# Kernel optimization log

Hardware: AMD Instinct MI355X
Metric: run time of the kernel (lower is better)

The kernel has to match this reference:

```python
import jax, jax.numpy as jnp
import numpy as np

N, E, D_IN, D_H, D_OUT, L = 100000, 300000, 128, 128, 3, 12


def _gconv(x, edges, W0, b0, W1, b1):
    # pytorch3d GraphConv: w0(x) + gather_scatter(w1(x), edges)
    y = x @ W0.T + b0                      # [N, D_out] self transform
    n = x @ W1.T + b1                      # [N, D_out] neighbor transform
    # undirected: each edge (i, j) adds n[j] to out[i] and n[i] to out[j]
    agg = jnp.zeros_like(y)
    agg = agg.at[edges[:, 0]].add(n[edges[:, 1]])
    agg = agg.at[edges[:, 1]].add(n[edges[:, 0]])
    return y + agg


def setup_inputs() -> dict:
    key = jax.random.key(0)
    ks = jax.random.split(key, 20)

    def lin(k, out_d, in_d):
        s = 1.0 / np.sqrt(in_d)
        return jax.random.uniform(k, (out_d, in_d), jnp.float32, -s, s)

    def bias(k, out_d, in_d):
        s = 1.0 / np.sqrt(in_d)
        return jax.random.uniform(k, (out_d,), jnp.float32, -s, s)

    features = jax.random.normal(ks[0], (N, D_IN), jnp.float32)
    edges = jax.random.randint(ks[1], (E, 2), 0, N, dtype=jnp.int32)

    # first layer (in -> hidden)
    W0_1, b0_1 = lin(ks[2], D_H, D_IN), bias(ks[3], D_H, D_IN)
    W1_1, b1_1 = lin(ks[4], D_H, D_IN), bias(ks[5], D_H, D_IN)
    # 12 hidden layers (hidden -> hidden), stacked for lax.scan
    W0_h = jax.vmap(lambda k: lin(k, D_H, D_H))(jax.random.split(ks[6], L))
    b0_h = jax.vmap(lambda k: bias(k, D_H, D_H))(jax.random.split(ks[7], L))
    W1_h = jax.vmap(lambda k: lin(k, D_H, D_H))(jax.random.split(ks[8], L))
    b1_h = jax.vmap(lambda k: bias(k, D_H, D_H))(jax.random.split(ks[9], L))
    # last layer (hidden -> out)
    W0_l, b0_l = lin(ks[10], D_OUT, D_H), bias(ks[11], D_OUT, D_H)
    W1_l, b1_l = lin(ks[12], D_OUT, D_H), bias(ks[13], D_OUT, D_H)

    return {
        "features": features, "edges": edges,
        "W0_1": W0_1, "b0_1": b0_1, "W1_1": W1_1, "b1_1": b1_1,
        "W0_h": W0_h, "b0_h": b0_h, "W1_h": W1_h, "b1_h": b1_h,
        "W0_l": W0_l, "b0_l": b0_l, "W1_l": W1_l, "b1_l": b1_l,
    }


def reference(features, edges, W0_1, b0_1, W1_1, b1_1,
              W0_h, b0_h, W1_h, b1_h, W0_l, b0_l, W1_l, b1_l):
    x = jax.nn.relu(_gconv(features, edges, W0_1, b0_1, W1_1, b1_1))
    residual = x

    def step(x, p):
        W0, b0, W1, b1 = p
        return jax.nn.relu(_gconv(x, edges, W0, b0, W1, b1)), None

    x, _ = jax.lax.scan(step, x, (W0_h, b0_h, W1_h, b1_h))
    auxiliary = x
    vertices = _gconv(residual + x, edges, W0_l, b0_l, W1_l, b1_l)
    return vertices, auxiliary
```

## Files before the change

### kernel.cpp

```cpp
#include <hip/hip_runtime.h>
#include <hip/hip_bf16.h>

#define D 128
#define OSTR 136
#define CHUNK 12544

typedef float f32x4  __attribute__((ext_vector_type(4)));
typedef unsigned int u32x4 __attribute__((ext_vector_type(4)));
typedef __attribute__((ext_vector_type(8))) __bf16 bh8;

union UV { uint4 u; bh8 h; };

__device__ inline float bf2f(unsigned short u) {
    union { unsigned int i; float f; } x; x.i = ((unsigned int)u) << 16; return x.f;
}
__device__ inline unsigned short f2bf(float f) {
    union { float f; unsigned int i; } x; x.f = f;
    return (unsigned short)((x.i + 0x7fffu + ((x.i >> 16) & 1u)) >> 16);
}
__device__ inline unsigned int addb2(unsigned int ua, unsigned int ub) {
    union { unsigned int i; float f; } la, ha, lb, hb;
    la.i = ua << 16; ha.i = ua & 0xffff0000u;
    lb.i = ub << 16; hb.i = ub & 0xffff0000u;
    return ((unsigned int)f2bf(ha.f + hb.f) << 16) | f2bf(la.f + lb.f);
}

__global__ void k_hist(const int* __restrict__ edges, int E, int* __restrict__ deg) {
    int e = blockIdx.x * blockDim.x + threadIdx.x;
    if (e < E) {
        atomicAdd(&deg[edges[2 * e]], 1);
        atomicAdd(&deg[edges[2 * e + 1]], 1);
    }
}

__global__ void k_scan1(const int* __restrict__ deg, int n,
                        int* __restrict__ incl, int* __restrict__ bsum) {
    __shared__ int lds[1024];
    int t = threadIdx.x;
    int i = blockIdx.x * 1024 + t;
    int v = (i < n) ? deg[i] : 0;
    int cur = v;
    lds[t] = cur;
    __syncthreads();
    for (int off = 1; off < 1024; off <<= 1) {
        int add = (t >= off) ? lds[t - off] : 0;
        __syncthreads();
        cur += add;
        lds[t] = cur;
        __syncthreads();
    }
    if (i < n) incl[i] = cur;
    if (t == 1023) bsum[blockIdx.x] = cur;
}

__global__ void k_scan2(int* __restrict__ bsum, int nb) {
    __shared__ int lds[128];
    int t = threadIdx.x;
    int v = (t < nb) ? bsum[t] : 0;
    int cur = v;
    lds[t] = cur;
    __syncthreads();
    for (int off = 1; off < 128; off <<= 1) {
        int add = (t >= off) ? lds[t - off] : 0;
        __syncthreads();
        cur += add;
        lds[t] = cur;
        __syncthreads();
    }
    if (t < nb) bsum[t] = cur - v;
}

__global__ void k_scan3(const int* __restrict__ incl, const int* __restrict__ deg,
                        const int* __restrict__ bsum, int n, int twoE,
                        int* __restrict__ rowstart, int* __restrict__ cursor) {
    int i = blockIdx.x * blockDim.x + threadIdx.x;
    if (i < n) {
        int r = incl[i] - deg[i] + bsum[i >> 10];
        rowstart[i] = r;
        cursor[i] = r;
    }
    if (i == 0) rowstart[n] = twoE;
}

__global__ void k_fill(const int* __restrict__ edges, int E,
                       int* __restrict__ cursor, int* __restrict__ adj) {
    int e = blockIdx.x * blockDim.x + threadIdx.x;
    if (e < E) {
        int a = edges[2 * e], b = edges[2 * e + 1];
        adj[atomicAdd(&cursor[a], 1)] = b;
        adj[atomicAdd(&cursor[b], 1)] = a;
    }
}

__global__ void k_wprep(const float* __restrict__ W0_1, const float* __restrict__ W1_1,
                        const float* __restrict__ W0_h, const float* __restrict__ W1_h,
                        unsigned short* __restrict__ wb) {
    int idx = blockIdx.x * 256 + threadIdx.x;
    if (idx >= 13 * 2 * 128 * 128) return;
    int k = idx & 127;
    int o = (idx >> 7) & 127;
    int m = (idx >> 14) & 1;
    int l = idx >> 15;
    const float* src = (l == 0) ? (m ? W1_1 : W0_1)
                                : ((m ? W1_h : W0_h) + (size_t)(l - 1) * 16384);
    float v = src[o * 128 + k];
    int kk = m * 128 + k;
    wb[(size_t)l * 32768 + (kk >> 5) * 4096 + o * 32 + (kk & 31)] = f2bf(v);
}

__global__ void k_cvt(const float* __restrict__ in, unsigned short* __restrict__ out, int n4) {
    int i = blockIdx.x * blockDim.x + threadIdx.x;
    if (i >= n4) return;
    f32x4 v = *(const f32x4*)&in[(size_t)i * 4];
    unsigned short u[4];
    #pragma unroll
    for (int j = 0; j < 4; ++j) u[j] = f2bf(v[j]);
    *(uint2*)&out[(size_t)i * 4] = *(uint2*)u;
}

__global__ __launch_bounds__(256) void k_agg(
    const unsigned short* __restrict__ x, const int* __restrict__ rowstart,
    const int* __restrict__ adj, unsigned short* __restrict__ s, int n) {
    int node = (blockIdx.x & 7) * CHUNK + (blockIdx.x >> 3) * 4 + (threadIdx.x >> 6);
    int lane = threadIdx.x & 63;
    if (node >= n) return;
    int r0 = rowstart[node], r1 = rowstart[node + 1];
    int c  = lane & 31;
    int hi = lane >> 5;
    float aa0 = 0.f, aa1 = 0.f, aa2 = 0.f, aa3 = 0.f;
    for (int p = r0; p < r1; p += 8) {
        int q = p + (lane & 7);
        int idx = (q < r1) ? adj[q] : adj[r0];
        uint2 u[4];
        #pragma unroll
        for (int k = 0; k < 4; ++k) {
            int j = __shfl(idx, 2 * k + hi);
            u[k] = *(const uint2*)&x[(size_t)j * D + c * 4];
        }
        #pragma unroll
        for (int k = 0; k < 4; ++k) {
            if (p + 2 * k + hi < r1) {
                union { unsigned int i; float f; } t;
                t.i = u[k].x << 16;          aa0 += t.f;
                t.i = u[k].x & 0xffff0000u;  aa1 += t.f;
                t.i = u[k].y << 16;          aa2 += t.f;
                t.i = u[k].y & 0xffff0000u;  aa3 += t.f;
            }
        }
    }
    aa0 += __shfl_xor(aa0, 32);
    aa1 += __shfl_xor(aa1, 32);
    aa2 += __shfl_xor(aa2, 32);
    aa3 += __shfl_xor(aa3, 32);
    if (hi == 0) {
        uint2 o;
        o.x = ((unsigned int)f2bf(aa1) << 16) | f2bf(aa0);
        o.y = ((unsigned int)f2bf(aa3) << 16) | f2bf(aa2);
        *(uint2*)&s[(size_t)node * D + c * 4] = o;
    }
}

__global__ __launch_bounds__(256) void k_gemm(
    const unsigned short* __restrict__ x,
    const unsigned short* __restrict__ s,
    const unsigned short* __restrict__ wb,
    const float* __restrict__ b0, const float* __restrict__ b1,
    const int* __restrict__ deg,
    unsigned short* __restrict__ out,
    float* __restrict__ out32,
    const unsigned short* __restrict__ resid,
    unsigned short* __restrict__ zout,
    int n, int do_relu) {
    __shared__ __align__(16) unsigned short LDS[64 * OSTR];
    int node0 = (blockIdx.x & 7) * CHUNK + (blockIdx.x >> 3) * 64;
    if (node0 >= n) return;
    int t = threadIdx.x;
    int lane = t & 63;
    int wave = t >> 6;
    int wm = (wave >> 1) * 32;
    int wn = (wave & 1) * 64;
    int mlane = lane & 15;
    int quad = lane >> 4;

    f32x4 acc[2][4];
    #pragma unroll
    for (int i = 0; i < 2; ++i)
        #pragma unroll
        for (int j = 0; j < 4; ++j) acc[i][j] = (f32x4){0.f, 0.f, 0.f, 0.f};

    uint4 ra[2][2];
    bh8 rb[2][4];
    auto LDK = [&](int kc, int st) {
        const unsigned short* srcA = (kc < 4) ? x : s;
        int kbase = (kc & 3) * 32;
        #pragma unroll
        for (int i = 0; i < 2; ++i) {
            int g = node0 + wm + i * 16 + mlane;
            uint4 v = {0u, 0u, 0u, 0u};
            if (g < n) v = *(const uint4*)&srcA[(size_t)g * D + kbase + quad * 8];
            ra[st][i] = v;
        }
        #pragma unroll
        for (int j = 0; j < 4; ++j)
            rb[st][j] = *(const bh8*)&wb[(size_t)kc * 4096 + (wn + j * 16 + mlane) * 32 + quad * 8];
    };

    LDK(0, 0);
    #pragma unroll
    for (int kc = 0; kc < 8; ++kc) {
        int cs = kc & 1;
        if (kc < 7) LDK(kc + 1, cs ^ 1);
        bh8 a0, a1;
        { UV v; v.u = ra[cs][0]; a0 = v.h; }
        { UV v; v.u = ra[cs][1]; a1 = v.h; }
        #pragma unroll
        for (int j = 0; j < 4; ++j) {
            acc[0][j] = __builtin_amdgcn_mfma_f32_16x16x32_bf16(a0, rb[cs][j], acc[0][j], 0, 0, 0);
            acc[1][j] = __builtin_amdgcn_mfma_f32_16x16x32_bf16(a1, rb[cs][j], acc[1][j], 0, 0, 0);
        }
    }

    #pragma unroll
    for (int i = 0; i < 2; ++i) {
        int mrow = wm + i * 16 + quad * 4;
        #pragma unroll
        for (int j = 0; j < 4; ++j) {
            int nn = wn + j * 16 + mlane;
            float b0v = b0[nn], b1v = b1[nn];
            #pragma unroll
            for (int r = 0; r < 4; ++r) {
                int g = node0 + mrow + r;
                float dg = (g < n) ? (float)deg[g] : 0.f;
                float val = acc[i][j][r] + b0v + dg * b1v;
                if (do_relu) val = fmaxf(val, 0.f);
                LDS[(mrow + r) * OSTR + nn] = f2bf(val);
            }
        }
    }
    __syncthreads();
    #pragma unroll
    for (int pass = 0; pass < 4; ++pass) {
        int row = pass * 16 + (t >> 4);
        int seg = (t & 15) * 8;
        int g = node0 + row;
        if (g < n) {
            u32x4 v = *(const u32x4*)&LDS[row * OSTR + seg];
            *(u32x4*)&out[(size_t)g * D + seg] = v;
            if (zout) {
                u32x4 rr = *(const u32x4*)&resid[(size_t)g * D + seg];
                u32x4 zz;
                zz.x = addb2(v.x, rr.x);
                zz.y = addb2(v.y, rr.y);
                zz.z = addb2(v.z, rr.z);
                zz.w = addb2(v.w, rr.w);
                *(u32x4*)&zout[(size_t)g * D + seg] = zz;
            }
        }
    }
    if (out32) {
        #pragma unroll
        for (int pass = 0; pass < 8; ++pass) {
            int row = pass * 8 + (t >> 5);
            int seg = (t & 31) * 4;
            int g = node0 + row;
            if (g < n) {
                f32x4 v;
                #pragma unroll
                for (int j = 0; j < 4; ++j) v[j] = bf2f(LDS[row * OSTR + seg + j]);
                *(f32x4*)&out32[(size_t)g * D + seg] = v;
            }
        }
    }
}

__global__ __launch_bounds__(256) void k_lastagg(
    const unsigned short* __restrict__ z, const int* __restrict__ rowstart,
    const int* __restrict__ adj,
    const float* __restrict__ W0, const float* __restrict__ b0,
    const float* __restrict__ W1, const float* __restrict__ b1,
    float* __restrict__ vert, int n) {
    int node = blockIdx.x * 4 + (threadIdx.x >> 6);
    int lane = threadIdx.x & 63;
    if (node >= n) return;
    int r0 = rowstart[node], r1 = rowstart[node + 1];
    int c  = lane & 31;
    int hi = lane >> 5;
    float aa0 = 0.f, aa1 = 0.f, aa2 = 0.f, aa3 = 0.f;
    for (int p = r0; p < r1; p += 8) {
        int q = p + (lane & 7);
        int idx = (q < r1) ? adj[q] : adj[r0];
        uint2 u[4];
        #pragma unroll
        for (int k = 0; k < 4; ++k) {
            int j = __shfl(idx, 2 * k + hi);
            u[k] = *(const uint2*)&z[(size_t)j * D + c * 4];
        }
        #pragma unroll
        for (int k = 0; k < 4; ++k) {
            if (p + 2 * k + hi < r1) {
                union { unsigned int i; float f; } t;
                t.i = u[k].x << 16;          aa0 += t.f;
                t.i = u[k].x & 0xffff0000u;  aa1 += t.f;
                t.i = u[k].y << 16;          aa2 += t.f;
                t.i = u[k].y & 0xffff0000u;  aa3 += t.f;
            }
        }
    }
    aa0 += __shfl_xor(aa0, 32);
    aa1 += __shfl_xor(aa1, 32);
    aa2 += __shfl_xor(aa2, 32);
    aa3 += __shfl_xor(aa3, 32);
    uint2 zz = *(const uint2*)&z[(size_t)node * D + c * 4];
    float z0, z1, z2, z3;
    { union { unsigned int i; float f; } t;
      t.i = zz.x << 16;         z0 = t.f;
      t.i = zz.x & 0xffff0000u; z1 = t.f;
      t.i = zz.y << 16;         z2 = t.f;
      t.i = zz.y & 0xffff0000u; z3 = t.f; }
    float dg = (float)(r1 - r0);
    #pragma unroll
    for (int o = 0; o < 3; ++o) {
        f32x4 w0 = *(const f32x4*)&W0[o * D + 4 * c];
        f32x4 w1 = *(const f32x4*)&W1[o * D + 4 * c];
        float p = z0 * w0[0] + z1 * w0[1] + z2 * w0[2] + z3 * w0[3]
                + aa0 * w1[0] + aa1 * w1[1] + aa2 * w1[2] + aa3 * w1[3];
        p += __shfl_xor(p, 16);
        p += __shfl_xor(p, 8);
        p += __shfl_xor(p, 4);
        p += __shfl_xor(p, 2);
        p += __shfl_xor(p, 1);
        if (lane == 0) vert[(size_t)node * 3 + o] = p + b0[o] + dg * b1[o];
    }
}

extern "C" void kernel_launch(void* const* d_in, const int* in_sizes, int n_in,
                              void* d_out, int out_size, void* d_ws, size_t ws_size,
                              hipStream_t stream) {
    const float* features = (const float*)d_in[0];
    const int*   edges    = (const int*)d_in[1];
    const float* W0_1 = (const float*)d_in[2];
    const float* b0_1 = (const float*)d_in[3];
    const float* W1_1 = (const float*)d_in[4];
    const float* b1_1 = (const float*)d_in[5];
    const float* W0_h = (const float*)d_in[6];
    const float* b0_h = (const float*)d_in[7];
    const float* W1_h = (const float*)d_in[8];
    const float* b1_h = (const float*)d_in[9];
    const float* W0_l = (const float*)d_in[10];
    const float* b0_l = (const float*)d_in[11];
    const float* W1_l = (const float*)d_in[12];
    const float* b1_l = (const float*)d_in[13];

    const int N_ = 100000, E_ = 300000;
    float* vert = (float*)d_out;
    float* aux  = (float*)d_out + (size_t)N_ * 3;

    char* w = (char*)d_ws;
    auto alloc = [&](size_t bytes) {
        char* p = w;
        w += (bytes + 255) & ~(size_t)255;
        return p;
    };
    unsigned short* wb    = (unsigned short*)alloc((size_t)13 * 32768 * 2);
    unsigned short* xf    = (unsigned short*)alloc((size_t)N_ * D * 2);
    unsigned short* resid = (unsigned short*)alloc((size_t)N_ * D * 2);
    unsigned short* xa    = (unsigned short*)alloc((size_t)N_ * D * 2);
    unsigned short* xb    = (unsigned short*)alloc((size_t)N_ * D * 2);
    unsigned short* sb    = (unsigned short*)alloc((size_t)N_ * D * 2);
    int* deg    = (int*)alloc((size_t)N_ * 4);
    int* incl   = (int*)alloc((size_t)N_ * 4);
    int* rowst  = (int*)alloc((size_t)(N_ + 1) * 4);
    int* cursor = (int*)alloc((size_t)N_ * 4);
    int* bsum   = (int*)alloc(128 * 4);
    int* adj    = (int*)alloc((size_t)2 * E_ * 4);

    hipMemsetAsync(deg, 0, (size_t)N_ * 4, stream);
    k_hist<<<(E_ + 255) / 256, 256, 0, stream>>>(edges, E_, deg);
    int nb = (N_ + 1023) / 1024;
    k_scan1<<<nb, 1024, 0, stream>>>(deg, N_, incl, bsum);
    k_scan2<<<1, 128, 0, stream>>>(bsum, nb);
    k_scan3<<<(N_ + 255) / 256, 256, 0, stream>>>(incl, deg, bsum, N_, 2 * E_, rowst, cursor);
    k_fill<<<(E_ + 255) / 256, 256, 0, stream>>>(edges, E_, cursor, adj);

    k_wprep<<<(13 * 2 * 16384 + 255) / 256, 256, 0, stream>>>(W0_1, W1_1, W0_h, W1_h, wb);
    k_cvt<<<(N_ * D / 4 + 255) / 256, 256, 0, stream>>>(features, xf, N_ * D / 4);

    int gblocks = 8 * ((CHUNK) / 64);
    int ablocks = 8 * ((CHUNK) / 4);
    int lblocks = (N_ + 3) / 4;

    k_agg<<<ablocks, 256, 0, stream>>>(xf, rowst, adj, sb, N_);
    k_gemm<<<gblocks, 256, 0, stream>>>(xf, sb, wb, b0_1, b1_1, deg, resid,
                                        nullptr, nullptr, nullptr, N_, 1);

    for (int h = 0; h < 12; ++h) {
        const unsigned short* in = (h == 0) ? resid : ((h & 1) ? xa : xb);
        unsigned short* outp = (h & 1) ? xb : xa;
        float* o32 = (h == 11) ? aux : nullptr;
        const unsigned short* radd = (h == 11) ? resid : nullptr;
        unsigned short* zo = (h == 11) ? xf : nullptr;
        k_agg<<<ablocks, 256, 0, stream>>>(in, rowst, adj, sb, N_);
        k_gemm<<<gblocks, 256, 0, stream>>>(in, sb, wb + (size_t)(1 + h) * 32768,
                                            b0_h + h * 128, b1_h + h * 128, deg,
                                            outp, o32, radd, zo, N_, 1);
    }

    k_lastagg<<<lblocks, 256, 0, stream>>>(xf, rowst, adj, W0_l, b0_l, W1_l, b1_l,
                                           vert, N_);
}
```

Baseline: 1.165 ms.

## Fuse neighbor aggregation into GEMM kernel via LDS staging

Merges the separate gather-aggregation kernel into the GEMM kernel. Each wave aggregates neighbor sums for 16 nodes into shared memory, and the GEMM then reads its second K-half from LDS instead of a global buffer. This removes one launch per layer and the write and re-read of the aggregated N×128 bf16 buffer. In exchange, the per-node gather is serialized within each wave (16 nodes sequentially), so there is less parallelism for hiding gather latency, and a barrier is added before the epilogue reuses LDS.

```diff
diff --git a/kernel.cpp b/kernel.cpp
--- a/kernel.cpp
+++ b/kernel.cpp
@@ -2,7 +2,7 @@
 #include <hip/hip_bf16.h>
 
 #define D 128
-#define OSTR 136
+#define SSTR 136
 #define CHUNK 12544
 
 typedef float f32x4  __attribute__((ext_vector_type(4)));
@@ -118,65 +118,71 @@
     *(uint2*)&out[(size_t)i * 4] = *(uint2*)u;
 }
 
-__global__ __launch_bounds__(256) void k_agg(
-    const unsigned short* __restrict__ x, const int* __restrict__ rowstart,
-    const int* __restrict__ adj, unsigned short* __restrict__ s, int n) {
-    int node = (blockIdx.x & 7) * CHUNK + (blockIdx.x >> 3) * 4 + (threadIdx.x >> 6);
-    int lane = threadIdx.x & 63;
-    if (node >= n) return;
-    int r0 = rowstart[node], r1 = rowstart[node + 1];
-    int c  = lane & 31;
-    int hi = lane >> 5;
-    float aa0 = 0.f, aa1 = 0.f, aa2 = 0.f, aa3 = 0.f;
-    for (int p = r0; p < r1; p += 8) {
-        int q = p + (lane & 7);
-        int idx = (q < r1) ? adj[q] : adj[r0];
-        uint2 u[4];
-        #pragma unroll
-        for (int k = 0; k < 4; ++k) {
-            int j = __shfl(idx, 2 * k + hi);
-            u[k] = *(const uint2*)&x[(size_t)j * D + c * 4];
-        }
-        #pragma unroll
-        for (int k = 0; k < 4; ++k) {
-            if (p + 2 * k + hi < r1) {
-                union { unsigned int i; float f; } t;
-                t.i = u[k].x << 16;          aa0 += t.f;
-                t.i = u[k].x & 0xffff0000u;  aa1 += t.f;
-                t.i = u[k].y << 16;          aa2 += t.f;
-                t.i = u[k].y & 0xffff0000u;  aa3 += t.f;
-            }
-        }
-    }
-    aa0 += __shfl_xor(aa0, 32);
-    aa1 += __shfl_xor(aa1, 32);
-    aa2 += __shfl_xor(aa2, 32);
-    aa3 += __shfl_xor(aa3, 32);
-    if (hi == 0) {
-        uint2 o;
-        o.x = ((unsigned int)f2bf(aa1) << 16) | f2bf(aa0);
-        o.y = ((unsigned int)f2bf(aa3) << 16) | f2bf(aa2);
-        *(uint2*)&s[(size_t)node * D + c * 4] = o;
-    }
-}
-
-__global__ __launch_bounds__(256) void k_gemm(
+__global__ __launch_bounds__(256) void k_fused(
     const unsigned short* __restrict__ x,
-    const unsigned short* __restrict__ s,
     const unsigned short* __restrict__ wb,
     const float* __restrict__ b0, const float* __restrict__ b1,
+    const int* __restrict__ rowstart, const int* __restrict__ adj,
     const int* __restrict__ deg,
     unsigned short* __restrict__ out,
     float* __restrict__ out32,
     const unsigned short* __restrict__ resid,
     unsigned short* __restrict__ zout,
     int n, int do_relu) {
-    __shared__ __align__(16) unsigned short LDS[64 * OSTR];
+    __shared__ __align__(16) unsigned short LDS[64 * SSTR];
     int node0 = (blockIdx.x & 7) * CHUNK + (blockIdx.x >> 3) * 64;
     if (node0 >= n) return;
     int t = threadIdx.x;
     int lane = t & 63;
     int wave = t >> 6;
+
+    {
+        int first = node0 + wave * 16;
+        int cnt = n - first; if (cnt > 16) cnt = 16;
+        if (cnt > 0) {
+            int rl = lane; if (rl > cnt) rl = cnt;
+            int rsv = rowstart[first + rl];
+            int c  = lane & 31;
+            int hi = lane >> 5;
+            for (int i = 0; i < cnt; ++i) {
+                int r0 = __shfl(rsv, i);
+                int r1 = __shfl(rsv, i + 1);
+                float aa0 = 0.f, aa1 = 0.f, aa2 = 0.f, aa3 = 0.f;
+                for (int p = r0; p < r1; p += 8) {
+                    int q = p + (lane & 7);
+                    int idx = (q < r1) ? adj[q] : adj[r0];
+                    uint2 u[4];
+                    #pragma unroll
+                    for (int k = 0; k < 4; ++k) {
+                        int j = __shfl(idx, 2 * k + hi);
+                        u[k] = *(const uint2*)&x[(size_t)j * D + c * 4];
+                    }
+                    #pragma unroll
+                    for (int k = 0; k < 4; ++k) {
+                        if (p + 2 * k + hi < r1) {
+                            union { unsigned int i; float f; } tt;
+                            tt.i = u[k].x << 16;          aa0 += tt.f;
+                            tt.i = u[k].x & 0xffff0000u;  aa1 += tt.f;
+                            tt.i = u[k].y << 16;          aa2 += tt.f;
+                            tt.i = u[k].y & 0xffff0000u;  aa3 += tt.f;
+                        }
+                    }
+                }
+                aa0 += __shfl_xor(aa0, 32);
+                aa1 += __shfl_xor(aa1, 32);
+                aa2 += __shfl_xor(aa2, 32);
+                aa3 += __shfl_xor(aa3, 32);
+                if (hi == 0) {
+                    uint2 o;
+                    o.x = ((unsigned int)f2bf(aa1) << 16) | f2bf(aa0);
+                    o.y = ((unsigned int)f2bf(aa3) << 16) | f2bf(aa2);
+                    *(uint2*)&LDS[(wave * 16 + i) * SSTR + c * 4] = o;
+                }
+            }
+        }
+    }
+    __syncthreads();
+
     int wm = (wave >> 1) * 32;
     int wn = (wave & 1) * 64;
     int mlane = lane & 15;
@@ -191,14 +197,17 @@
     uint4 ra[2][2];
     bh8 rb[2][4];
     auto LDK = [&](int kc, int st) {
-        const unsigned short* srcA = (kc < 4) ? x : s;
-        int kbase = (kc & 3) * 32;
         #pragma unroll
         for (int i = 0; i < 2; ++i) {
-            int g = node0 + wm + i * 16 + mlane;
-            uint4 v = {0u, 0u, 0u, 0u};
-            if (g < n) v = *(const uint4*)&srcA[(size_t)g * D + kbase + quad * 8];
-            ra[st][i] = v;
+            int r = wm + i * 16 + mlane;
+            if (kc < 4) {
+                int g = node0 + r;
+                uint4 v = {0u, 0u, 0u, 0u};
+                if (g < n) v = *(const uint4*)&x[(size_t)g * D + (kc & 3) * 32 + quad * 8];
+                ra[st][i] = v;
+            } else {
+                ra[st][i] = *(const uint4*)&LDS[r * SSTR + (kc - 4) * 32 + quad * 8];
+            }
         }
         #pragma unroll
         for (int j = 0; j < 4; ++j)
@@ -220,6 +229,7 @@
         }
     }
 
+    __syncthreads();
     #pragma unroll
     for (int i = 0; i < 2; ++i) {
         int mrow = wm + i * 16 + quad * 4;
@@ -233,7 +243,7 @@
                 float dg = (g < n) ? (float)deg[g] : 0.f;
                 float val = acc[i][j][r] + b0v + dg * b1v;
                 if (do_relu) val = fmaxf(val, 0.f);
-                LDS[(mrow + r) * OSTR + nn] = f2bf(val);
+                LDS[(mrow + r) * SSTR + nn] = f2bf(val);
             }
         }
     }
@@ -244,7 +254,7 @@
         int seg = (t & 15) * 8;
         int g = node0 + row;
         if (g < n) {
-            u32x4 v = *(const u32x4*)&LDS[row * OSTR + seg];
+            u32x4 v = *(const u32x4*)&LDS[row * SSTR + seg];
             *(u32x4*)&out[(size_t)g * D + seg] = v;
             if (zout) {
                 u32x4 rr = *(const u32x4*)&resid[(size_t)g * D + seg];
@@ -266,7 +276,7 @@
             if (g < n) {
                 f32x4 v;
                 #pragma unroll
-                for (int j = 0; j < 4; ++j) v[j] = bf2f(LDS[row * OSTR + seg + j]);
+                for (int j = 0; j < 4; ++j) v[j] = bf2f(LDS[row * SSTR + seg + j]);
                 *(f32x4*)&out32[(size_t)g * D + seg] = v;
             }
         }
@@ -366,7 +376,6 @@
     unsigned short* resid = (unsigned short*)alloc((size_t)N_ * D * 2);
     unsigned short* xa    = (unsigned short*)alloc((size_t)N_ * D * 2);
     unsigned short* xb    = (unsigned short*)alloc((size_t)N_ * D * 2);
-    unsigned short* sb    = (unsigned short*)alloc((size_t)N_ * D * 2);
     int* deg    = (int*)alloc((size_t)N_ * 4);
     int* incl   = (int*)alloc((size_t)N_ * 4);
     int* rowst  = (int*)alloc((size_t)(N_ + 1) * 4);
@@ -386,12 +395,10 @@
     k_cvt<<<(N_ * D / 4 + 255) / 256, 256, 0, stream>>>(features, xf, N_ * D / 4);
 
     int gblocks = 8 * ((CHUNK) / 64);
-    int ablocks = 8 * ((CHUNK) / 4);
     int lblocks = (N_ + 3) / 4;
 
-    k_agg<<<ablocks, 256, 0, stream>>>(xf, rowst, adj, sb, N_);
-    k_gemm<<<gblocks, 256, 0, stream>>>(xf, sb, wb, b0_1, b1_1, deg, resid,
-                                        nullptr, nullptr, nullptr, N_, 1);
+    k_fused<<<gblocks, 256, 0, stream>>>(xf, wb, b0_1, b1_1, rowst, adj, deg,
+                                         resid, nullptr, nullptr, nullptr, N_, 1);
 
     for (int h = 0; h < 12; ++h) {
         const unsigned short* in = (h == 0) ? resid : ((h & 1) ? xa : xb);
@@ -399,10 +406,9 @@
         float* o32 = (h == 11) ? aux : nullptr;
         const unsigned short* radd = (h == 11) ? resid : nullptr;
         unsigned short* zo = (h == 11) ? xf : nullptr;
-        k_agg<<<ablocks, 256, 0, stream>>>(in, rowst, adj, sb, N_);
-        k_gemm<<<gblocks, 256, 0, stream>>>(in, sb, wb + (size_t)(1 + h) * 32768,
-                                            b0_h + h * 128, b1_h + h * 128, deg,
-                                            outp, o32, radd, zo, N_, 1);
+        k_fused<<<gblocks, 256, 0, stream>>>(in, wb + (size_t)(1 + h) * 32768,
+                                             b0_h + h * 128, b1_h + h * 128,
+                                             rowst, adj, deg, outp, o32, radd, zo, N_, 1);
     }
 
     k_lastagg<<<lblocks, 256, 0, stream>>>(xf, rowst, adj, W0_l, b0_l, W1_l, b1_l,
```

Measured after the change: 1.214 ms. +4.2%, slower.
